# Kernel optimization log

Hardware: AMD Instinct MI355X
Metric: run time of the kernel (lower is better)

## Reference

```python
import jax, jax.numpy as jnp
import numpy as np

B = 1_048_576
W = 64  # hidden width
N_FREQ = 6   # 3 dims * 6 freqs * (sin,cos) = 36
K_BLOB = 4   # one-blob bins per dim


def _freq_embed(p):
    # [B,3] -> [B,36]
    freqs = 2.0 ** jnp.arange(N_FREQ, dtype=p.dtype)
    ang = jnp.pi * p[:, :, None] * freqs  # [B,3,6]
    return jnp.concatenate([jnp.sin(ang), jnp.cos(ang)], axis=-1).reshape(p.shape[0], 3 * 2 * N_FREQ)


def _sph(d):
    # unit-square parameterization of a direction, [B,3] -> [B,2]
    d = d / (jnp.linalg.norm(d, axis=-1, keepdims=True) + 1e-8)
    u = jnp.arctan2(d[:, 1], d[:, 0]) / (2.0 * jnp.pi) + 0.5
    v = jnp.arccos(jnp.clip(d[:, 2], -1.0 + 1e-6, 1.0 - 1e-6)) / jnp.pi
    return jnp.stack([u, v], axis=-1)


def _one_blob(x, k=K_BLOB):
    # x in [0,1], [B,D] -> [B,D*k] Gaussian one-blob encoding
    centers = (jnp.arange(k, dtype=x.dtype) + 0.5) / k
    sigma = 1.0 / k
    g = jnp.exp(-0.5 * ((x[..., None] - centers) / sigma) ** 2)  # [B,D,k]
    return g.reshape(x.shape[0], -1)


def _encode(p, wi, n, alpha, beta, r):
    ones = jnp.ones((p.shape[0], 2), dtype=p.dtype)
    return jnp.concatenate([
        _freq_embed(p),                      # 36
        _one_blob(_sph(wi)),                 # 8
        _one_blob(_sph(n)),                  # 8
        _one_blob(1.0 - jnp.exp(-r)),        # 4
        alpha, beta,                         # 6
        ones,                                # 2 (implicit bias)
    ], axis=-1)                              # -> [B,64]


def _mlp(x, Ws):
    h = x
    for Wk in Ws[:-1]:
        h = jax.nn.relu(h @ Wk.T)
    return h @ Ws[-1].T  # [B,3]


def setup_inputs() -> dict:
    key = jax.random.key(0)
    ks = jax.random.split(key, 13)
    p = jax.random.normal(ks[0], (B, 3), jnp.float32)
    wi = jax.random.normal(ks[1], (B, 3), jnp.float32)
    n = jax.random.normal(ks[2], (B, 3), jnp.float32)
    alpha = jax.random.uniform(ks[3], (B, 3), jnp.float32)
    beta = jax.random.uniform(ks[4], (B, 3), jnp.float32)
    r = jax.random.uniform(ks[5], (B, 1), jnp.float32)
    s = 1.0 / np.sqrt(W)
    weights = {}
    for i in range(6):
        weights[f"W{i}"] = jax.random.normal(ks[6 + i], (W, W), jnp.float32) * s
    weights["W6"] = jax.random.normal(ks[12], (3, W), jnp.float32) * s
    return dict(p=p, wi=wi, n=n, alpha=alpha, beta=beta, r=r, **weights)


def reference(p, wi, n, alpha, beta, r, W0, W1, W2, W3, W4, W5, W6):
    x = _encode(p, wi, n, alpha, beta, r)
    out = _mlp(x, [W0, W1, W2, W3, W4, W5, W6])
    return out * (alpha + beta)  # reflectance factorization
```

## Files before the change

kernel.cpp:

```cpp
#include <hip/hip_runtime.h>


typedef _Float16 f16;
typedef f16 f16x2 __attribute__((ext_vector_type(2)));
typedef f16 f16x4 __attribute__((ext_vector_type(4)));
typedef f16 f16x8 __attribute__((ext_vector_type(8)));
typedef float f32x4 __attribute__((ext_vector_type(4)));

#define MFMA32(A, B, C) __builtin_amdgcn_mfma_f32_16x16x32_f16(A, B, C, 0, 0, 0)
#define LDS_FENCE() __asm__ volatile("" ::: "memory")

static constexpr int TILES  = 4;
static constexpr int WAVES  = 4;
static constexpr int BLOCK  = WAVES * 64;
static constexpr int NB     = 8;
static constexpr int SPB    = WAVES * NB * 64;

static constexpr int    WUNITS   = 50;
static constexpr int    WCHUNKS  = WUNITS * 64;
static constexpr size_t WS_BYTES = (size_t)WCHUNKS * 16;
static constexpr int    LDSUNITS = 42;
static constexpr int    LDSCHNK  = LDSUNITS * 64;
static constexpr int    LDS_WEI  = LDSUNITS * 1024;
static constexpr int    LDS_STG  = WAVES * 8192;
static constexpr int    LDS_TOT  = LDS_WEI + LDS_STG;

__host__ __device__ __forceinline__ int tau(int x) {
    return (x & 32) + ((x & 7) >> 2) * 16 + ((x >> 3) & 3) * 4 + (x & 3);
}

__device__ __forceinline__ f16x2 pkh(float a, float b) {
    return __builtin_bit_cast(f16x2, __builtin_amdgcn_cvt_pkrtz(a, b));
}

__device__ __forceinline__ f16x4 cat22(f16x2 a, f16x2 b) {
    return __builtin_shufflevector(a, b, 0, 1, 2, 3);
}

__device__ __forceinline__ f16x8 cat44(f16x4 a, f16x4 b) {
    return __builtin_shufflevector(a, b, 0, 1, 2, 3, 4, 5, 6, 7);
}

__device__ __forceinline__ f16x4 pack4(f32x4 v) {
    return cat22(pkh(v[0], v[1]), pkh(v[2], v[3]));
}

__device__ __forceinline__ float fast_atan2_rev(float y, float x) {
    const float ax = __builtin_fabsf(x), ay = __builtin_fabsf(y);
    const float mx = fmaxf(ax, ay), mn = fminf(ax, ay);
    const float a = mn * __builtin_amdgcn_rcpf(fmaxf(mx, 1e-30f));
    const float s = a * a;
    float r = a * (0.99997726f + s * (-0.33262347f + s * (0.19354346f +
              s * (-0.11643287f + s * (0.05265332f - s * 0.01172120f)))));
    if (ay > ax) r = 1.5707963268f - r;
    if (x < 0.0f) r = 3.1415926536f - r;
    r = (y < 0.0f) ? -r : r;
    return r * 0.15915494309189535f;
}

__device__ __forceinline__ float fast_acos(float x) {
    const float ax = __builtin_fabsf(x);
    const float t = __builtin_amdgcn_sqrtf(1.0f - ax);
    const float p = t * (1.5707288f + ax * (-0.2121144f +
                    ax * (0.0742610f - ax * 0.0187293f)));
    return (x < 0.0f) ? (3.1415926536f - p) : p;
}

__device__ __forceinline__ void blob4(float x, float* out) {
    const float dx = x - 0.125f;
    const float E0 = __expf(-8.0f * dx * dx);
    const float R  = __expf(4.0f * dx);
    const float t1 = R * 0.60653066f;
    const float t2 = R * 0.22313016f;
    const float t3 = R * 0.082084999f;
    out[0] = E0;
    out[1] = E0 * t1;
    out[2] = out[1] * t2;
    out[3] = out[2] * t3;
}

__device__ __forceinline__ f16x8 make_wchunk(
    int c, const float* __restrict__ W0, const float* __restrict__ W1,
    const float* __restrict__ W2, const float* __restrict__ W3,
    const float* __restrict__ W4, const float* __restrict__ W5,
    const float* __restrict__ W6)
{
    const int lane2 = c & 63;
    const int unit  = c >> 6;
    const int q = lane2 >> 4, m = lane2 & 15;
    f16x8 v;
    if (unit < 48) {
        const int l = unit >> 3, kt = (unit & 7) >> 2, mt = unit & 3;
        const float* Ws[6] = {W0, W1, W2, W3, W4, W5};
        const float* __restrict__ Wl = Ws[l];
#pragma unroll
        for (int j = 0; j < 8; ++j) {
            const int x = kt * 32 + q * 8 + j;
            const int src = (l == 0) ? x : tau(x);
            v[j] = (f16)Wl[(mt * 16 + m) * 64 + src];
        }
    } else {
        const int kt = unit - 48;
#pragma unroll
        for (int j = 0; j < 8; ++j) {
            const int src = tau(kt * 32 + q * 8 + j);
            v[j] = (m < 3) ? (f16)W6[m * 64 + src] : (f16)0.0f;
        }
    }
    return v;
}

__global__ __launch_bounds__(256, 1) void pack_weights_kernel(
    const float* __restrict__ W0, const float* __restrict__ W1,
    const float* __restrict__ W2, const float* __restrict__ W3,
    const float* __restrict__ W4, const float* __restrict__ W5,
    const float* __restrict__ W6, f16* __restrict__ ws)
{
    const int c = (int)blockIdx.x * 256 + threadIdx.x;
    if (c >= WCHUNKS) return;
    *(f16x8*)(ws + (size_t)c * 8) = make_wchunk(c, W0, W1, W2, W3, W4, W5, W6);
}

__device__ __forceinline__ void async_ld16(const void* g, void* l) {
    __builtin_amdgcn_global_load_lds(
        (const __attribute__((address_space(1))) void*)g,
        (__attribute__((address_space(3))) void*)l,
        16, 0, 0);
}

struct EncIn {
    float pv[3], wv[3], nv[3], av[3], bv[3], rv;
};

__device__ __forceinline__ EncIn load_inputs(
    const float* __restrict__ P,  const float* __restrict__ WI,
    const float* __restrict__ NV, const float* __restrict__ AL,
    const float* __restrict__ BE, const float* __restrict__ RR, int s)
{
    EncIn e;
#pragma unroll
    for (int d = 0; d < 3; ++d) {
        e.pv[d] = P [s * 3 + d];
        e.wv[d] = WI[s * 3 + d];
        e.nv[d] = NV[s * 3 + d];
        e.av[d] = AL[s * 3 + d];
        e.bv[d] = BE[s * 3 + d];
    }
    e.rv = RR[s];
    return e;
}

__device__ __forceinline__ void enc_slice(
    int k, const EncIn& e, unsigned char* myrow, int rot, float* abn)
{
    auto put = [&](int D, f16x2 a, f16x2 b) {
        *(f16x4*)(myrow + (((D + rot) & 31) << 2)) = cat22(a, b);
    };
    if (k <= 2) {
        const int d = k;
        float sA[6], cA[6];
        const float fr = __builtin_amdgcn_fractf(e.pv[d] * 0.5f);
        sA[0] = __builtin_amdgcn_sinf(fr);
        cA[0] = __builtin_amdgcn_cosf(fr);
#pragma unroll
        for (int kk = 1; kk < 6; ++kk) {
            const float s2 = sA[kk-1] * sA[kk-1];
            const float sc = sA[kk-1] * cA[kk-1];
            cA[kk] = fmaf(-2.0f, s2, 1.0f);
            sA[kk] = sc + sc;
        }
        put(6*d + 0, pkh(sA[0], sA[1]), pkh(sA[2], sA[3]));
        put(6*d + 2, pkh(sA[4], sA[5]), pkh(cA[0], cA[1]));
        put(6*d + 4, pkh(cA[2], cA[3]), pkh(cA[4], cA[5]));
    } else if (k <= 4) {
        const int which = k - 3;
        const float dx = which ? e.nv[0] : e.wv[0];
        const float dy = which ? e.nv[1] : e.wv[1];
        const float dz = which ? e.nv[2] : e.wv[2];
        const int D0 = 18 + which * 4;
        const float nr = __builtin_amdgcn_sqrtf(dx*dx + dy*dy + dz*dz) + 1e-8f;
        const float u  = fast_atan2_rev(dy, dx) + 0.5f;
        float zc = dz * __builtin_amdgcn_rcpf(nr);
        zc = fminf(fmaxf(zc, -1.0f + 1e-6f), 1.0f - 1e-6f);
        const float vv = fast_acos(zc) * 0.3183098861837907f;
        float ob[8];
        blob4(u,  &ob[0]);
        blob4(vv, &ob[4]);
        put(D0,     pkh(ob[0], ob[1]), pkh(ob[2], ob[3]));
        put(D0 + 2, pkh(ob[4], ob[5]), pkh(ob[6], ob[7]));
    } else {
        float ob[4];
        blob4(1.0f - __expf(-e.rv), ob);
        put(26, pkh(ob[0], ob[1]), pkh(ob[2], ob[3]));
        put(28, pkh(e.av[0], e.av[1]), pkh(e.av[2], e.bv[0]));
        put(30, pkh(e.bv[1], e.bv[2]), pkh(1.0f, 1.0f));
        abn[0] = e.av[0] + e.bv[0];
        abn[1] = e.av[1] + e.bv[1];
        abn[2] = e.av[2] + e.bv[2];
    }
}

template<int PACKED>
__global__ __launch_bounds__(BLOCK, 2) void nrc_mlp_kernel(
    const float* __restrict__ P,  const float* __restrict__ WI,
    const float* __restrict__ NV, const float* __restrict__ AL,
    const float* __restrict__ BE, const float* __restrict__ RR,
    const f16*   __restrict__ ws,
    const float* __restrict__ W0, const float* __restrict__ W1,
    const float* __restrict__ W2, const float* __restrict__ W3,
    const float* __restrict__ W4, const float* __restrict__ W5,
    const float* __restrict__ W6, float* __restrict__ Out)
{
    __shared__ __attribute__((aligned(16))) unsigned char smem[LDS_TOT];

    const int tid  = threadIdx.x;
    const int lane = tid & 63;
    const int w    = tid >> 6;
    const int q    = lane >> 4;
    const int m    = lane & 15;
    const int wave_base = (int)blockIdx.x * SPB + w * (NB * 64);

    unsigned char* const stgw  = smem + LDS_WEI + w * 8192;
    unsigned char* const myrow = stgw + lane * 128;
    const int rot = (lane * 4) & 31;
    unsigned char* const wbl   = smem + lane * 16;

    if (PACKED) {
#pragma unroll
        for (int i = 0; i < (LDSCHNK + BLOCK - 1) / BLOCK; ++i) {
            const int c = i * BLOCK + tid;
            if (c < LDSCHNK)
                async_ld16(ws + (size_t)(512 + c) * 8, smem + c * 16);
        }
    } else {
#pragma unroll
        for (int i = 0; i < (LDSCHNK + BLOCK - 1) / BLOCK; ++i) {
            const int c = i * BLOCK + tid;
            if (c < LDSCHNK)
                *(f16x8*)(smem + c * 16) =
                    make_wchunk(512 + c, W0, W1, W2, W3, W4, W5, W6);
        }
    }

    f16x8 w0f[8];
    if (PACKED) {
#pragma unroll
        for (int f = 0; f < 8; ++f)
            w0f[f] = *(const f16x8*)(ws + (size_t)(f * 64 + lane) * 8);
    } else {
#pragma unroll
        for (int f = 0; f < 8; ++f)
            w0f[f] = make_wchunk(f * 64 + lane, W0, W1, W2, W3, W4, W5, W6);
    }

    float ab_cur[3], abn[3];
    {
        EncIn e0 = load_inputs(P, WI, NV, AL, BE, RR, wave_base + lane);
#pragma unroll
        for (int k = 0; k < 6; ++k)
            enc_slice(k, e0, myrow, rot, abn);
        ab_cur[0] = abn[0]; ab_cur[1] = abn[1]; ab_cur[2] = abn[2];
    }

    __syncthreads();

    const f16x4 zero4 = {(f16)0.0f, (f16)0.0f, (f16)0.0f, (f16)0.0f};
    const f32x4 ZF = {0.0f, 0.0f, 0.0f, 0.0f};

    f16x8 bf[TILES][2];
    LDS_FENCE();
#pragma unroll
    for (int t = 0; t < TILES; ++t)
#pragma unroll
        for (int kt = 0; kt < 2; ++kt) {
            const int s0 = (16 * kt + 4 * q + 4 * m) & 31;
            bf[t][kt] = *(const f16x8*)(stgw + (t * 16 + m) * 128 + (s0 << 2));
        }
    LDS_FENCE();

    EncIn cur = load_inputs(P, WI, NV, AL, BE, RR, wave_base + 64 + lane);
    EncIn nxt = cur;

#pragma unroll 1
    for (int b = 0; b < NB; ++b) {
        const bool hn = (b + 1 < NB);
        if (b + 2 < NB)
            nxt = load_inputs(P, WI, NV, AL, BE, RR,
                              wave_base + (b + 2) * 64 + lane);

        f32x4 acc[TILES][4];
#pragma unroll
        for (int layer = 0; layer < 6; ++layer) {
            f16x8 wa[4];
            __builtin_amdgcn_s_setprio(1);
            if (layer == 0) {
#pragma unroll
                for (int mt = 0; mt < 4; ++mt) wa[mt] = w0f[mt];
            } else {
#pragma unroll
                for (int mt = 0; mt < 4; ++mt)
                    wa[mt] = *(const f16x8*)(wbl + ((layer - 1) * 8 + mt) * 1024);
            }
#pragma unroll
            for (int t = 0; t < TILES; ++t)
#pragma unroll
                for (int mt = 0; mt < 4; ++mt)
                    acc[t][mt] = MFMA32(wa[mt], bf[t][0], ZF);
            if (layer == 0) {
#pragma unroll
                for (int mt = 0; mt < 4; ++mt) wa[mt] = w0f[4 + mt];
            } else {
#pragma unroll
                for (int mt = 0; mt < 4; ++mt)
                    wa[mt] = *(const f16x8*)(wbl + ((layer - 1) * 8 + 4 + mt) * 1024);
            }
#pragma unroll
            for (int t = 0; t < TILES; ++t)
#pragma unroll
                for (int mt = 0; mt < 4; ++mt)
                    acc[t][mt] = MFMA32(wa[mt], bf[t][1], acc[t][mt]);
            __builtin_amdgcn_s_setprio(0);

            if (hn) enc_slice(layer, cur, myrow, rot, abn);

#pragma unroll
            for (int t = 0; t < TILES; ++t) {
                f16x4 pk[4];
#pragma unroll
                for (int mt = 0; mt < 4; ++mt)
                    pk[mt] = __builtin_elementwise_max(pack4(acc[t][mt]), zero4);
                bf[t][0] = cat44(pk[0], pk[1]);
                bf[t][1] = cat44(pk[2], pk[3]);
            }
        }

        {
            const int rbase = wave_base + b * 64;
            f32x4 oz[TILES];
            const f16x8 w6a = *(const f16x8*)(wbl + 40 * 1024);
#pragma unroll
            for (int t = 0; t < TILES; ++t) oz[t] = MFMA32(w6a, bf[t][0], ZF);
            const f16x8 w6b = *(const f16x8*)(wbl + 41 * 1024);
#pragma unroll
            for (int t = 0; t < TILES; ++t) oz[t] = MFMA32(w6b, bf[t][1], oz[t]);
#pragma unroll
            for (int t = 0; t < TILES; ++t) {
                const float s0 = __shfl(ab_cur[0], t * 16 + m);
                const float s1 = __shfl(ab_cur[1], t * 16 + m);
                const float s2 = __shfl(ab_cur[2], t * 16 + m);
                if (lane < 16) {
                    const int s = rbase + t * 16 + m;
                    float* o = Out + s * 3;
                    o[0] = oz[t][0] * s0;
                    o[1] = oz[t][1] * s1;
                    o[2] = oz[t][2] * s2;
                }
            }
        }

        if (hn) {
            ab_cur[0] = abn[0]; ab_cur[1] = abn[1]; ab_cur[2] = abn[2];
            LDS_FENCE();
#pragma unroll
            for (int t = 0; t < TILES; ++t)
#pragma unroll
                for (int kt = 0; kt < 2; ++kt) {
                    const int s0 = (16 * kt + 4 * q + 4 * m) & 31;
                    bf[t][kt] = *(const f16x8*)(
                        stgw + (t * 16 + m) * 128 + (s0 << 2));
                }
            LDS_FENCE();
            cur = nxt;
        }
    }
}

extern "C" void kernel_launch(void* const* d_in, const int* in_sizes, int n_in,
                              void* d_out, int out_size, void* d_ws, size_t ws_size,
                              hipStream_t stream) {
    (void)n_in; (void)out_size;
    const float* P  = (const float*)d_in[0];
    const float* WI = (const float*)d_in[1];
    const float* NV = (const float*)d_in[2];
    const float* AL = (const float*)d_in[3];
    const float* BE = (const float*)d_in[4];
    const float* RR = (const float*)d_in[5];
    const float* W0 = (const float*)d_in[6];
    const float* W1 = (const float*)d_in[7];
    const float* W2 = (const float*)d_in[8];
    const float* W3 = (const float*)d_in[9];
    const float* W4 = (const float*)d_in[10];
    const float* W5 = (const float*)d_in[11];
    const float* W6 = (const float*)d_in[12];
    f16*   ws  = (f16*)d_ws;
    float* Out = (float*)d_out;

    const int Bn = in_sizes[0] / 3;
    const int grid = Bn / SPB;

    if (ws_size >= WS_BYTES) {
        hipLaunchKernelGGL(pack_weights_kernel, dim3((WCHUNKS + 255) / 256),
                           dim3(256), 0, stream, W0, W1, W2, W3, W4, W5, W6, ws);
        hipLaunchKernelGGL((nrc_mlp_kernel<1>), dim3(grid), dim3(BLOCK), 0, stream,
                           P, WI, NV, AL, BE, RR, ws,
                           W0, W1, W2, W3, W4, W5, W6, Out);
    } else {
        hipLaunchKernelGGL((nrc_mlp_kernel<0>), dim3(grid), dim3(BLOCK), 0, stream,
                           P, WI, NV, AL, BE, RR, ws,
                           W0, W1, W2, W3, W4, W5, W6, Out);
    }
}
```

Measured before the change: 160.3 us.

## Software-pipeline layer weight fragments from LDS and keep W6 in registers

Moves W0 into LDS alongside the other hidden layers and keeps W6 fragments resident in registers instead of W0. Weight fragments for the next layer are prefetched from LDS into double-buffered registers (wcur/wnxt) while the current layer's MFMAs run. The ReLU/pack step is folded into the start of each tile's next-layer MFMA sequence so packing interleaves with matrix work. This grows LDS use by six units (more shared memory per block, possibly lower occupancy) in exchange for hiding LDS weight-load latency.

```diff
diff --git a/kernel.cpp b/kernel.cpp
--- a/kernel.cpp
+++ b/kernel.cpp
@@ -19,7 +19,7 @@
 static constexpr int    WUNITS   = 50;
 static constexpr int    WCHUNKS  = WUNITS * 64;
 static constexpr size_t WS_BYTES = (size_t)WCHUNKS * 16;
-static constexpr int    LDSUNITS = 42;
+static constexpr int    LDSUNITS = 48;
 static constexpr int    LDSCHNK  = LDSUNITS * 64;
 static constexpr int    LDS_WEI  = LDSUNITS * 1024;
 static constexpr int    LDS_STG  = WAVES * 8192;
@@ -222,35 +222,31 @@
 
     unsigned char* const stgw  = smem + LDS_WEI + w * 8192;
     unsigned char* const myrow = stgw + lane * 128;
-    const int rot = (lane * 4) & 31;
+    const int rot = (4 * lane) & 31;
     unsigned char* const wbl   = smem + lane * 16;
 
     if (PACKED) {
 #pragma unroll
-        for (int i = 0; i < (LDSCHNK + BLOCK - 1) / BLOCK; ++i) {
+        for (int i = 0; i < LDSCHNK / BLOCK; ++i) {
             const int c = i * BLOCK + tid;
-            if (c < LDSCHNK)
-                async_ld16(ws + (size_t)(512 + c) * 8, smem + c * 16);
+            async_ld16(ws + (size_t)c * 8, smem + c * 16);
         }
     } else {
 #pragma unroll
-        for (int i = 0; i < (LDSCHNK + BLOCK - 1) / BLOCK; ++i) {
+        for (int i = 0; i < LDSCHNK / BLOCK; ++i) {
             const int c = i * BLOCK + tid;
-            if (c < LDSCHNK)
-                *(f16x8*)(smem + c * 16) =
-                    make_wchunk(512 + c, W0, W1, W2, W3, W4, W5, W6);
-        }
-    }
-
-    f16x8 w0f[8];
+            *(f16x8*)(smem + c * 16) =
+                make_wchunk(c, W0, W1, W2, W3, W4, W5, W6);
+        }
+    }
+
+    f16x8 w6a, w6b;
     if (PACKED) {
-#pragma unroll
-        for (int f = 0; f < 8; ++f)
-            w0f[f] = *(const f16x8*)(ws + (size_t)(f * 64 + lane) * 8);
+        w6a = *(const f16x8*)(ws + (size_t)(3072 + lane) * 8);
+        w6b = *(const f16x8*)(ws + (size_t)(3136 + lane) * 8);
     } else {
-#pragma unroll
-        for (int f = 0; f < 8; ++f)
-            w0f[f] = make_wchunk(f * 64 + lane, W0, W1, W2, W3, W4, W5, W6);
+        w6a = make_wchunk(3072 + lane, W0, W1, W2, W3, W4, W5, W6);
+        w6b = make_wchunk(3136 + lane, W0, W1, W2, W3, W4, W5, W6);
     }
 
     float ab_cur[3], abn[3];
@@ -266,6 +262,14 @@
 
     const f16x4 zero4 = {(f16)0.0f, (f16)0.0f, (f16)0.0f, (f16)0.0f};
     const f32x4 ZF = {0.0f, 0.0f, 0.0f, 0.0f};
+
+    f16x8 wcur[4], wnxt[4];
+#pragma unroll
+    for (int mt = 0; mt < 4; ++mt)
+        wcur[mt] = *(const f16x8*)(wbl + mt * 1024);
+#pragma unroll
+    for (int mt = 0; mt < 4; ++mt)
+        wnxt[mt] = *(const f16x8*)(wbl + (4 + mt) * 1024);
 
     f16x8 bf[TILES][2];
     LDS_FENCE();
@@ -291,38 +295,45 @@
         f32x4 acc[TILES][4];
 #pragma unroll
         for (int layer = 0; layer < 6; ++layer) {
-            f16x8 wa[4];
             __builtin_amdgcn_s_setprio(1);
-            if (layer == 0) {
-#pragma unroll
-                for (int mt = 0; mt < 4; ++mt) wa[mt] = w0f[mt];
-            } else {
+#pragma unroll
+            for (int t = 0; t < TILES; ++t) {
+                if (layer > 0) {
+                    f16x4 pk[4];
+#pragma unroll
+                    for (int mt = 0; mt < 4; ++mt)
+                        pk[mt] = __builtin_elementwise_max(pack4(acc[t][mt]), zero4);
+                    bf[t][0] = cat44(pk[0], pk[1]);
+                    bf[t][1] = cat44(pk[2], pk[3]);
+                }
 #pragma unroll
                 for (int mt = 0; mt < 4; ++mt)
-                    wa[mt] = *(const f16x8*)(wbl + ((layer - 1) * 8 + mt) * 1024);
+                    acc[t][mt] = MFMA32(wcur[mt], bf[t][0], ZF);
             }
+            __builtin_amdgcn_s_setprio(0);
+            {
+                const int nl = (layer + 1) % 6;
+#pragma unroll
+                for (int mt = 0; mt < 4; ++mt)
+                    wcur[mt] = *(const f16x8*)(wbl + (nl * 8 + mt) * 1024);
+            }
+            if (hn) enc_slice(layer, cur, myrow, rot, abn);
+            __builtin_amdgcn_s_setprio(1);
 #pragma unroll
             for (int t = 0; t < TILES; ++t)
 #pragma unroll
                 for (int mt = 0; mt < 4; ++mt)
-                    acc[t][mt] = MFMA32(wa[mt], bf[t][0], ZF);
-            if (layer == 0) {
-#pragma unroll
-                for (int mt = 0; mt < 4; ++mt) wa[mt] = w0f[4 + mt];
-            } else {
+                    acc[t][mt] = MFMA32(wnxt[mt], bf[t][1], acc[t][mt]);
+            __builtin_amdgcn_s_setprio(0);
+            {
+                const int nl = (layer + 1) % 6;
 #pragma unroll
                 for (int mt = 0; mt < 4; ++mt)
-                    wa[mt] = *(const f16x8*)(wbl + ((layer - 1) * 8 + 4 + mt) * 1024);
+                    wnxt[mt] = *(const f16x8*)(wbl + (nl * 8 + 4 + mt) * 1024);
             }
-#pragma unroll
-            for (int t = 0; t < TILES; ++t)
-#pragma unroll
-                for (int mt = 0; mt < 4; ++mt)
-                    acc[t][mt] = MFMA32(wa[mt], bf[t][1], acc[t][mt]);
-            __builtin_amdgcn_s_setprio(0);
-
-            if (hn) enc_slice(layer, cur, myrow, rot, abn);
-
+        }
+
+        {
 #pragma unroll
             for (int t = 0; t < TILES; ++t) {
                 f16x4 pk[4];
@@ -332,15 +343,10 @@
                 bf[t][0] = cat44(pk[0], pk[1]);
                 bf[t][1] = cat44(pk[2], pk[3]);
             }
-        }
-
-        {
             const int rbase = wave_base + b * 64;
             f32x4 oz[TILES];
-            const f16x8 w6a = *(const f16x8*)(wbl + 40 * 1024);
 #pragma unroll
             for (int t = 0; t < TILES; ++t) oz[t] = MFMA32(w6a, bf[t][0], ZF);
-            const f16x8 w6b = *(const f16x8*)(wbl + 41 * 1024);
 #pragma unroll
             for (int t = 0; t < TILES; ++t) oz[t] = MFMA32(w6b, bf[t][1], oz[t]);
 #pragma unroll
```

After: 157.1 us. 1.02x faster.
